# Optimization experiments

Hardware: AMD Instinct MI355X
Metric: run time of the kernel (lower is better)

The kernel has to match this reference:

```python
import jax, jax.numpy as jnp
import numpy as np


def _ln(x, g, b, eps=1e-5):
    mu = x.mean(-1, keepdims=True)
    var = ((x - mu) ** 2).mean(-1, keepdims=True)
    return (x - mu) / jnp.sqrt(var + eps) * g + b


def setup_inputs() -> dict:
    key = jax.random.key(0)
    ks = jax.random.split(key, 12)
    B, H, W, nh = 32, 64, 64, 8
    L = H * W
    dim, ffn_dim, mem_dim = 512, 2048, 512
    s = 0.02
    d = {}
    d["query"] = jax.random.normal(ks[0], (B, 1, dim), jnp.float32)
    d["mem"] = jax.random.normal(ks[1], (B, L, mem_dim), jnp.float32)
    d["ior_embs"] = jax.random.uniform(ks[2], (B, nh, H, W), jnp.float32)
    # input_proj: Linear(mem_dim, dim) + ReLU + LayerNorm(dim)
    d["W_in"] = jax.random.normal(ks[3], (mem_dim, dim), jnp.float32) * s
    d["b_in"] = jnp.zeros((dim,), jnp.float32)
    d["g_in"] = jnp.ones((dim,), jnp.float32)
    d["be_in"] = jnp.zeros((dim,), jnp.float32)
    # q_w: Linear(dim, dim); kv_w: Linear(dim, 2*dim)
    d["Wq"] = jax.random.normal(ks[4], (dim, dim), jnp.float32) * s
    d["bq"] = jnp.zeros((dim,), jnp.float32)
    d["Wkv"] = jax.random.normal(ks[5], (dim, 2 * dim), jnp.float32) * s
    d["bkv"] = jnp.zeros((2 * dim,), jnp.float32)
    # ffn: Mlp(dim, ffn_dim, dim) with GELU (exact)
    d["W1"] = jax.random.normal(ks[6], (dim, ffn_dim), jnp.float32) * s
    d["b1"] = jnp.zeros((ffn_dim,), jnp.float32)
    d["W2"] = jax.random.normal(ks[7], (ffn_dim, dim), jnp.float32) * s
    d["b2"] = jnp.zeros((dim,), jnp.float32)
    # norm_q, norm_ffn LayerNorms
    d["g_q"] = jnp.ones((dim,), jnp.float32)
    d["be_q"] = jnp.zeros((dim,), jnp.float32)
    d["g_f"] = jnp.ones((dim,), jnp.float32)
    d["be_f"] = jnp.zeros((dim,), jnp.float32)
    return d


def reference(query, mem, ior_embs, W_in, b_in, g_in, be_in, Wq, bq, Wkv, bkv,
              W1, b1, W2, b2, g_q, be_q, g_f, be_f):
    # input_proj: Linear + ReLU + LayerNorm
    m = _ln(jax.nn.relu(mem @ W_in + b_in), g_in, be_in)  # [B,L,C]
    B, L, C = m.shape
    nh = ior_embs.shape[1]
    h = C // nh
    scale = h ** -0.5
    ior = ior_embs.reshape(B, nh, L)  # flatten(2)
    kv = m @ Wkv + bkv
    k, v = kv[..., :C], kv[..., C:]
    # per-head split along last dim == reshape to [.., nh, h]
    q = (_ln(query, g_q, be_q) @ Wq + bq).reshape(B, 1, nh, h)
    k = k.reshape(B, L, nh, h)
    v = v.reshape(B, L, nh, h)
    # softmax-free attention gated by ior mask: attn = (q@k^T)*scale*ior
    attn = jnp.einsum('bqhd,blhd->bhql', q, k) * scale * ior[:, :, None, :]  # [B,nh,1,L]
    x = jnp.einsum('bhql,blhd->bqhd', attn, v).reshape(B, 1, C)  # concat heads
    x = x + query  # residual (short_cut)
    # FFN with pre-norm; dropout p=0 -> identity
    hdn = jax.nn.gelu(_ln(x, g_f, be_f) @ W1 + b1, approximate=False)
    x = x + (hdn @ W2 + b2)
    return x
```

## Files before the change

### kernel.cpp

```cpp
#include <hip/hip_runtime.h>
#include <hip/hip_bf16.h>
#include <math.h>

typedef unsigned short u16;
typedef __bf16 bf16x8 __attribute__((ext_vector_type(8)));
typedef float f32x4 __attribute__((ext_vector_type(4)));

__device__ __forceinline__ float b2f(u16 u) {
  union { unsigned int i; float f; } v; v.i = ((unsigned int)u) << 16; return v.f;
}
__device__ __forceinline__ u16 f2b(float f) {
  union { float f; unsigned int i; } v; v.f = f;
  unsigned int x = v.i;
  return (u16)((x + 0x7fffu + ((x >> 16) & 1u)) >> 16);
}
__device__ __forceinline__ float ldx(const void* p, size_t i, int isf) {
  return isf ? ((const float*)p)[i] : b2f(((const u16*)p)[i]);
}

__global__ void k_detect(const void* __restrict__ query, int* __restrict__ flag) {
  int t = threadIdx.x;
  float v = ((const float*)query)[t];
  int ok = (v == v && fabsf(v) < 100.f && fabsf(v) > 1e-4f) ? 1 : 0;
  unsigned long long m = __ballot(ok);
  if (t == 0) flag[0] = (__popcll(m) >= 32) ? 1 : 0;
}

__global__ __launch_bounds__(256) void k_makeB(const void* __restrict__ Win,
                                               u16* __restrict__ WTf,
                                               const int* __restrict__ flag) {
  int isf = flag[0];
  int t = threadIdx.x;
  int bx = blockIdx.x & 7, by = blockIdx.x >> 3;
  int k0 = bx * 64, j0 = by * 64;
  __shared__ float tile[64][65];
  #pragma unroll
  for (int kx = 0; kx < 16; kx++) {
    int idx = t + 256 * kx;
    int kl = idx >> 6, jl = idx & 63;
    tile[kl][jl] = ldx(Win, (size_t)(k0 + kl) * 512 + (j0 + jl), isf);
  }
  __syncthreads();
  #pragma unroll
  for (int i = 0; i < 2; i++) {
    int chunk = i * 256 + t;
    int q  = chunk & 3;
    int l  = (chunk >> 2) & 15;
    int ksL = (chunk >> 6) & 1;
    int jbL = (chunk >> 7) & 3;
    int j_local = jbL * 16 + l;
    int k_local = ksL * 32 + q * 8;
    union { u16 h[8]; uint4 u; } pk;
    #pragma unroll
    for (int r = 0; r < 8; r++) pk.h[r] = f2b(tile[k_local + r][j_local]);
    int jb = by * 4 + jbL, ks = bx * 2 + ksL;
    *(uint4*)(WTf + ((size_t)(jb * 16 + ks) * 16 + l) * 32 + q * 8) = pk.u;
  }
}

__global__ __launch_bounds__(512) void k_prep2(const void* __restrict__ Wkv,
                                               const void* __restrict__ g_in,
                                               const void* __restrict__ be_in,
                                               float* __restrict__ P1, float* __restrict__ P2,
                                               const int* __restrict__ flag) {
  int isf = flag[0];
  int blk = blockIdx.x;
  int t = threadIdx.x;
  int jj = t & 31, cg = t >> 5;
  int j = blk * 32 + jj;
  float p1 = 0.f, p2 = 0.f;
  for (int cc = 0; cc < 32; cc++) {
    int c = cg * 32 + cc;
    float wv = ldx(Wkv, (size_t)c * 1024 + 512 + j, isf);
    p1 += ldx(g_in, c, isf) * wv;
    p2 += ldx(be_in, c, isf) * wv;
  }
  __shared__ float red[1024];
  red[t * 2] = p1; red[t * 2 + 1] = p2;
  __syncthreads();
  if (t < 32) {
    float s1 = 0.f, s2 = 0.f;
    for (int g2 = 0; g2 < 16; g2++) { s1 += red[(g2 * 32 + t) * 2]; s2 += red[(g2 * 32 + t) * 2 + 1]; }
    P1[blk * 32 + t] = s1;
    P2[blk * 32 + t] = s2;
  }
}

__global__ __launch_bounds__(256) void k_qprep_a(
    const void* __restrict__ query, const void* __restrict__ Wq, const void* __restrict__ bq,
    const void* __restrict__ g_q, const void* __restrict__ be_q,
    float* __restrict__ qr_ws, const int* __restrict__ flag) {
  int isf = flag[0];
  int b = blockIdx.x, jq = blockIdx.y, t = threadIdx.x;
  __shared__ float qf[512];
  __shared__ float red[8];
  __shared__ float stats[2];

  float s = 0.f, ss = 0.f;
  for (int k = 0; k < 2; k++) {
    int c = t + 256 * k;
    float v = ldx(query, (size_t)b * 512 + c, isf);
    qf[c] = v; s += v; ss += v * v;
  }
  for (int off = 32; off; off >>= 1) { s += __shfl_xor(s, off); ss += __shfl_xor(ss, off); }
  int wid = t >> 6, lane = t & 63;
  if (lane == 0) { red[wid * 2] = s; red[wid * 2 + 1] = ss; }
  __syncthreads();
  if (t == 0) {
    float S = 0.f, SS = 0.f;
    for (int w = 0; w < 4; w++) { S += red[w * 2]; SS += red[w * 2 + 1]; }
    float mu = S / 512.f;
    float var = SS / 512.f - mu * mu;
    stats[0] = mu; stats[1] = rsqrtf(var + 1e-5f);
  }
  __syncthreads();
  float mu = stats[0], rstd = stats[1];
  for (int k = 0; k < 2; k++) {
    int c = t + 256 * k;
    qf[c] = (qf[c] - mu) * rstd * ldx(g_q, c, isf) + ldx(be_q, c, isf);
  }
  __syncthreads();
  int jl = t >> 1, half = t & 1;
  int j = jq * 128 + jl;
  const float* qh = qf + half * 256;
  float a0 = 0.f, a1 = 0.f, a2 = 0.f, a3 = 0.f;
  if (isf) {
    const float* wp = (const float*)Wq + (size_t)(half * 256) * 512 + j;
    #pragma unroll 2
    for (int cc = 0; cc < 256; cc += 4) {
      a0 += qh[cc]     * wp[(size_t)cc * 512];
      a1 += qh[cc + 1] * wp[(size_t)(cc + 1) * 512];
      a2 += qh[cc + 2] * wp[(size_t)(cc + 2) * 512];
      a3 += qh[cc + 3] * wp[(size_t)(cc + 3) * 512];
    }
  } else {
    const u16* wp = (const u16*)Wq + (size_t)(half * 256) * 512 + j;
    #pragma unroll 2
    for (int cc = 0; cc < 256; cc += 4) {
      a0 += qh[cc]     * b2f(wp[(size_t)cc * 512]);
      a1 += qh[cc + 1] * b2f(wp[(size_t)(cc + 1) * 512]);
      a2 += qh[cc + 2] * b2f(wp[(size_t)(cc + 2) * 512]);
      a3 += qh[cc + 3] * b2f(wp[(size_t)(cc + 3) * 512]);
    }
  }
  float acc = (a0 + a1) + (a2 + a3);
  acc += __shfl_xor(acc, 1);
  if (half == 0) qr_ws[(size_t)b * 512 + j] = acc + ldx(bq, j, isf);
}

__global__ __launch_bounds__(256) void k_qprep_b(
    const float* __restrict__ qr_ws, const void* __restrict__ Wkv, const void* __restrict__ bkv,
    const void* __restrict__ g_in, const void* __restrict__ be_in,
    u16* __restrict__ guT, float* __restrict__ Gsum_g, float* __restrict__ S0_g,
    const int* __restrict__ flag) {
  int isf = flag[0];
  int b = blockIdx.x, cq = blockIdx.y, t = threadIdx.x;
  __shared__ float qrl[512];
  __shared__ float ul[128 * 8];
  qrl[t] = qr_ws[(size_t)b * 512 + t];
  qrl[t + 256] = qr_ws[(size_t)b * 512 + t + 256];
  __syncthreads();
  #pragma unroll
  for (int e4 = 0; e4 < 4; e4++) {
    int e = t + 256 * e4;
    int cl = e >> 3, n = e & 7;
    int c = cq * 128 + cl;
    const float* qp = qrl + n * 64;
    float acc = 0.f;
    if (isf) {
      const float* wp = (const float*)Wkv + (size_t)c * 1024 + n * 64;
      #pragma unroll 8
      for (int d = 0; d < 64; d++) acc += wp[d] * qp[d];
    } else {
      const u16* wp = (const u16*)Wkv + (size_t)c * 1024 + n * 64;
      #pragma unroll 8
      for (int d = 0; d < 64; d++) acc += b2f(wp[d]) * qp[d];
    }
    ul[cl * 8 + n] = acc;
  }
  __syncthreads();
  #pragma unroll
  for (int e4 = 0; e4 < 4; e4++) {
    int e = t + 256 * e4;
    int cl = e >> 3, n = e & 7;
    int c = cq * 128 + cl;
    guT[((size_t)b * 16 + n) * 512 + c] = f2b(ldx(g_in, c, isf) * ul[cl * 8 + n]);
    guT[((size_t)b * 16 + 8 + n) * 512 + c] = 0;
  }
  if (t < 64) {
    int n = t >> 3, seg = t & 7;
    float gs = 0.f, s0 = 0.f;
    for (int k = 0; k < 16; k++) {
      int cl = seg * 16 + k;
      int c = cq * 128 + cl;
      float uu = ul[cl * 8 + n];
      gs += ldx(g_in, c, isf) * uu;
      s0 += ldx(be_in, c, isf) * uu;
    }
    gs += __shfl_xor(gs, 1); s0 += __shfl_xor(s0, 1);
    gs += __shfl_xor(gs, 2); s0 += __shfl_xor(s0, 2);
    gs += __shfl_xor(gs, 4); s0 += __shfl_xor(s0, 4);
    if (seg == 0) {
      atomicAdd(Gsum_g + b * 8 + n, gs);
      atomicAdd(S0_g + b * 8 + n, s0);
    }
  }
  if (cq == 0 && t < 8) {
    float acc = 0.f;
    for (int d = 0; d < 64; d++) acc += ldx(bkv, t * 64 + d, isf) * qrl[t * 64 + d];
    atomicAdd(S0_g + b * 8 + t, acc);
  }
}

#define LDA 40
__global__ __launch_bounds__(512) void k_main(
    const void* __restrict__ mem, const u16* __restrict__ WTf, const void* __restrict__ b_in,
    const void* __restrict__ ior, const u16* __restrict__ guT,
    const float* __restrict__ Gsum_g, const float* __restrict__ S0_g,
    float* __restrict__ R_g, float* __restrict__ A_g, float* __restrict__ M_g,
    const int* __restrict__ flag) {
  int isf = flag[0];
  int blk = blockIdx.x;
  int b   = blockIdx.y;
  int t = threadIdx.x;
  int w = t >> 6, lane = t & 63;
  int l15 = lane & 15, q = lane >> 4;

  __shared__ __align__(16) char smem[68096];
  u16*   Ab      = (u16*)smem;
  float* rowred  = (float*)smem;
  float* mu_rstd = (float*)(smem + 65536);
  float* a_lds   = (float*)(smem + 66048);
  char*  ymine   = smem + w * 8192;

  float binv[4];
  #pragma unroll
  for (int j = 0; j < 4; j++) binv[j] = ldx(b_in, w * 64 + j * 16 + l15, isf);
  bf16x8 gfrag0 = *(const bf16x8*)(guT + ((size_t)b * 16 + l15) * 512 + w * 64 + q * 8);
  bf16x8 gfrag1 = *(const bf16x8*)(guT + ((size_t)b * 16 + l15) * 512 + w * 64 + 32 + q * 8);
  float Gs  = Gsum_g[b * 8 + (t & 7)];
  float S0v = S0_g[b * 8 + (t & 7)];
  const u16* wb = WTf + (size_t)w * 32768 + l15 * 32 + q * 8;

  float am_acc = 0.f, mm_acc = 0.f;

  for (int tile = 0; tile < 4; tile++) {
    int row0 = (blk * 4 + tile) * 64;
    size_t memBase = ((size_t)b * 4096 + row0) * 512;

    f32x4 acc[4][4];
    #pragma unroll
    for (int i = 0; i < 4; i++)
      #pragma unroll
      for (int j = 0; j < 4; j++) { acc[i][j][0]=0.f; acc[i][j][1]=0.f; acc[i][j][2]=0.f; acc[i][j][3]=0.f; }

    for (int kk = 0; kk < 512; kk += 32) {
      __syncthreads();
      if (isf) {
        int e = t * 4;
        int r = e >> 5, c = e & 31;
        float4 v = *(const float4*)((const float*)mem + memBase + (size_t)r * 512 + kk + c);
        union { u16 h[4]; uint2 u; } pk;
        pk.h[0] = f2b(v.x); pk.h[1] = f2b(v.y); pk.h[2] = f2b(v.z); pk.h[3] = f2b(v.w);
        *(uint2*)(Ab + r * LDA + c) = pk.u;
      } else if (t < 256) {
        int r = t >> 2, ch = t & 3;
        uint4 v = *(const uint4*)((const u16*)mem + memBase + (size_t)r * 512 + kk + ch * 8);
        *(uint4*)(Ab + r * LDA + ch * 8) = v;
      }
      __syncthreads();
      int ks = kk >> 5;
      bf16x8 aF[4], bF[4];
      #pragma unroll
      for (int j = 0; j < 4; j++)
        bF[j] = *(const bf16x8*)(wb + j * 8192 + ks * 512);
      #pragma unroll
      for (int i = 0; i < 4; i++)
        aF[i] = *(const bf16x8*)(Ab + (i * 16 + l15) * LDA + q * 8);
      #pragma unroll
      for (int i = 0; i < 4; i++)
        #pragma unroll
        for (int j = 0; j < 4; j++)
          acc[i][j] = __builtin_amdgcn_mfma_f32_16x16x32_bf16(aF[i], bF[j], acc[i][j], 0, 0, 0);
    }
    __syncthreads();

    #pragma unroll
    for (int i = 0; i < 4; i++)
      #pragma unroll
      for (int j = 0; j < 4; j++)
        #pragma unroll
        for (int r = 0; r < 4; r++) {
          float v = acc[i][j][r] + binv[j];
          acc[i][j][r] = v > 0.f ? v : 0.f;
        }
    #pragma unroll
    for (int i = 0; i < 4; i++)
      #pragma unroll
      for (int r = 0; r < 4; r++) {
        float s  = acc[i][0][r] + acc[i][1][r] + acc[i][2][r] + acc[i][3][r];
        float ss = acc[i][0][r]*acc[i][0][r] + acc[i][1][r]*acc[i][1][r]
                 + acc[i][2][r]*acc[i][2][r] + acc[i][3][r]*acc[i][3][r];
        #pragma unroll
        for (int m = 1; m < 16; m <<= 1) { s += __shfl_xor(s, m); ss += __shfl_xor(ss, m); }
        if (l15 == 0) {
          int row = i * 16 + q * 4 + r;
          rowred[(w * 64 + row) * 2]     = s;
          rowred[(w * 64 + row) * 2 + 1] = ss;
        }
      }
    __syncthreads();
    if (t < 64) {
      float S = 0.f, SS = 0.f;
      for (int w2 = 0; w2 < 8; w2++) { S += rowred[(w2 * 64 + t) * 2]; SS += rowred[(w2 * 64 + t) * 2 + 1]; }
      float mu = S / 512.f;
      float var = SS / 512.f - mu * mu;
      mu_rstd[t * 2] = mu;
      mu_rstd[t * 2 + 1] = rsqrtf(var + 1e-5f);
    }
    __syncthreads();

    #pragma unroll
    for (int i = 0; i < 4; i++)
      #pragma unroll
      for (int j = 0; j < 4; j++)
        #pragma unroll
        for (int r = 0; r < 4; r++) {
          int row = i * 16 + q * 4 + r;
          int byo = (row * 128 + j * 32 + l15 * 2) ^ ((row & 7) << 4);
          *(u16*)(ymine + byo) = f2b(acc[i][j][r]);
        }
    __syncthreads();

    f32x4 Tacc[4];
    #pragma unroll
    for (int rt = 0; rt < 4; rt++) { Tacc[rt][0]=0.f; Tacc[rt][1]=0.f; Tacc[rt][2]=0.f; Tacc[rt][3]=0.f; }
    #pragma unroll
    for (int rt = 0; rt < 4; rt++) {
      int row = rt * 16 + l15;
      int sw = (row & 7) << 4;
      bf16x8 ay0 = *(const bf16x8*)(ymine + ((row * 128 + q * 16) ^ sw));
      Tacc[rt] = __builtin_amdgcn_mfma_f32_16x16x32_bf16(ay0, gfrag0, Tacc[rt], 0, 0, 0);
      bf16x8 ay1 = *(const bf16x8*)(ymine + ((row * 128 + 64 + q * 16) ^ sw));
      Tacc[rt] = __builtin_amdgcn_mfma_f32_16x16x32_bf16(ay1, gfrag1, Tacc[rt], 0, 0, 0);
    }
    {
      float* tp = (float*)ymine;
      if (l15 < 8) {
        #pragma unroll
        for (int rt = 0; rt < 4; rt++)
          #pragma unroll
          for (int r = 0; r < 4; r++)
            tp[(rt * 16 + q * 4 + r) * 8 + l15] = Tacc[rt][r];
      }
    }
    __syncthreads();

    {
      int row = t >> 3, n = t & 7;
      float Tsum = 0.f;
      #pragma unroll
      for (int w2 = 0; w2 < 8; w2++)
        Tsum += ((const float*)(smem + w2 * 8192))[row * 8 + n];
      float mu = mu_rstd[row * 2], rstd = mu_rstd[row * 2 + 1];
      float spre = rstd * (Tsum - mu * Gs) + S0v;
      float aval = spre * 0.125f * ldx(ior, ((size_t)b * 8 + n) * 4096 + row0 + row, isf);
      am_acc += aval;
      mm_acc += aval * mu * rstd;
      a_lds[row * 8 + n] = aval * rstd;
    }
    __syncthreads();

    float rv[4][8];
    #pragma unroll
    for (int j = 0; j < 4; j++)
      #pragma unroll
      for (int n = 0; n < 8; n++) rv[j][n] = 0.f;
    #pragma unroll
    for (int i = 0; i < 4; i++)
      #pragma unroll
      for (int r = 0; r < 4; r++) {
        int row = i * 16 + q * 4 + r;
        const float* ap = a_lds + row * 8;
        float a0=ap[0],a1=ap[1],a2=ap[2],a3=ap[3],a4=ap[4],a5=ap[5],a6=ap[6],a7=ap[7];
        #pragma unroll
        for (int j = 0; j < 4; j++) {
          float m = acc[i][j][r];
          rv[j][0] += m*a0; rv[j][1] += m*a1; rv[j][2] += m*a2; rv[j][3] += m*a3;
          rv[j][4] += m*a4; rv[j][5] += m*a5; rv[j][6] += m*a6; rv[j][7] += m*a7;
        }
      }
    #pragma unroll
    for (int j = 0; j < 4; j++)
      #pragma unroll
      for (int n = 0; n < 8; n++) {
        float v = rv[j][n];
        v += __shfl_xor(v, 16);
        v += __shfl_xor(v, 32);
        rv[j][n] = v;
      }
    if (q == 0) {
      #pragma unroll
      for (int j = 0; j < 4; j++)
        #pragma unroll
        for (int n = 0; n < 8; n++)
          atomicAdd(R_g + ((size_t)b * 8 + n) * 512 + (w * 64 + j * 16 + l15), rv[j][n]);
    }
  }

  am_acc += __shfl_xor(am_acc, 8);
  am_acc += __shfl_xor(am_acc, 16);
  am_acc += __shfl_xor(am_acc, 32);
  mm_acc += __shfl_xor(mm_acc, 8);
  mm_acc += __shfl_xor(mm_acc, 16);
  mm_acc += __shfl_xor(mm_acc, 32);
  if (lane < 8) {
    atomicAdd(A_g + b * 8 + lane, am_acc);
    atomicAdd(M_g + b * 8 + lane, mm_acc);
  }
}

__global__ __launch_bounds__(512) void k_mid(
    const float* __restrict__ R_g, const float* __restrict__ A_g, const float* __restrict__ M_g,
    const float* __restrict__ P1, const float* __restrict__ P2,
    const void* __restrict__ Wkv, const void* __restrict__ bkv, const void* __restrict__ g_in,
    const void* __restrict__ query, const void* __restrict__ g_f, const void* __restrict__ be_f,
    float* __restrict__ xrow_ws, float* __restrict__ xln_ws, float* __restrict__ y_acc,
    const int* __restrict__ flag) {
  int isf = flag[0];
  int b = blockIdx.x, t = threadIdx.x;
  __shared__ float Rl[4096];
  __shared__ float red[16];
  __shared__ float stats[2];
  #pragma unroll
  for (int k = 0; k < 8; k++) {
    int e = t + 512 * k;
    Rl[e] = R_g[(size_t)b * 4096 + e] * ldx(g_in, e & 511, isf);
  }
  __syncthreads();
  int j = t, n = t >> 6;
  float Av = A_g[b * 8 + n], Mv = M_g[b * 8 + n];
  float base = Av * ldx(bkv, 512 + j, isf) - Mv * P1[j] + Av * P2[j];
  const float* rl = Rl + n * 512;
  float a0 = 0.f, a1 = 0.f, a2 = 0.f, a3 = 0.f;
  if (isf) {
    const float* wv = (const float*)Wkv + 512 + j;
    #pragma unroll 2
    for (int c = 0; c < 512; c += 4) {
      a0 += rl[c]     * wv[(size_t)c * 1024];
      a1 += rl[c + 1] * wv[(size_t)(c + 1) * 1024];
      a2 += rl[c + 2] * wv[(size_t)(c + 2) * 1024];
      a3 += rl[c + 3] * wv[(size_t)(c + 3) * 1024];
    }
  } else {
    const u16* wv = (const u16*)Wkv + 512 + j;
    #pragma unroll 2
    for (int c = 0; c < 512; c += 4) {
      a0 += rl[c]     * b2f(wv[(size_t)c * 1024]);
      a1 += rl[c + 1] * b2f(wv[(size_t)(c + 1) * 1024]);
      a2 += rl[c + 2] * b2f(wv[(size_t)(c + 2) * 1024]);
      a3 += rl[c + 3] * b2f(wv[(size_t)(c + 3) * 1024]);
    }
  }
  float v = base + (a0 + a1) + (a2 + a3) + ldx(query, (size_t)b * 512 + t, isf);
  xrow_ws[(size_t)b * 512 + t] = v;
  y_acc[(size_t)b * 512 + t] = 0.f;
  float s1 = v, s2 = v * v;
  for (int off = 32; off; off >>= 1) { s1 += __shfl_xor(s1, off); s2 += __shfl_xor(s2, off); }
  int wid = t >> 6, lane = t & 63;
  if (lane == 0) { red[wid * 2] = s1; red[wid * 2 + 1] = s2; }
  __syncthreads();
  if (t == 0) {
    float S = 0.f, SS = 0.f;
    for (int w = 0; w < 8; w++) { S += red[w * 2]; SS += red[w * 2 + 1]; }
    float mu = S / 512.f;
    float var = SS / 512.f - mu * mu;
    stats[0] = mu; stats[1] = rsqrtf(var + 1e-5f);
  }
  __syncthreads();
  xln_ws[(size_t)b * 512 + t] = (v - stats[0]) * stats[1] * ldx(g_f, t, isf) + ldx(be_f, t, isf);
}

__global__ __launch_bounds__(512) void k_ffn12(
    const float* __restrict__ xln_ws, const void* __restrict__ W1, const void* __restrict__ b1,
    const void* __restrict__ W2, float* __restrict__ y_acc, const int* __restrict__ flag) {
  int isf = flag[0];
  int jb = blockIdx.x, b = blockIdx.y, t = threadIdx.x;
  __shared__ float xl[512];
  __shared__ float hl[512];
  xl[t] = xln_ws[(size_t)b * 512 + t];
  __syncthreads();
  int j = jb * 512 + t;
  float a0 = 0.f, a1 = 0.f, a2 = 0.f, a3 = 0.f;
  if (isf) {
    const float* wp = (const float*)W1 + j;
    #pragma unroll 2
    for (int c = 0; c < 512; c += 4) {
      a0 += xl[c]     * wp[(size_t)c * 2048];
      a1 += xl[c + 1] * wp[(size_t)(c + 1) * 2048];
      a2 += xl[c + 2] * wp[(size_t)(c + 2) * 2048];
      a3 += xl[c + 3] * wp[(size_t)(c + 3) * 2048];
    }
  } else {
    const u16* wp = (const u16*)W1 + j;
    #pragma unroll 2
    for (int c = 0; c < 512; c += 4) {
      a0 += xl[c]     * b2f(wp[(size_t)c * 2048]);
      a1 += xl[c + 1] * b2f(wp[(size_t)(c + 1) * 2048]);
      a2 += xl[c + 2] * b2f(wp[(size_t)(c + 2) * 2048]);
      a3 += xl[c + 3] * b2f(wp[(size_t)(c + 3) * 2048]);
    }
  }
  float acc = (a0 + a1) + (a2 + a3) + ldx(b1, j, isf);
  hl[t] = 0.5f * acc * (1.0f + erff(acc * 0.70710678118654752f));
  __syncthreads();
  float s0 = 0.f, s1 = 0.f, s2 = 0.f, s3 = 0.f;
  if (isf) {
    const float* wp = (const float*)W2 + (size_t)jb * 512 * 512 + t;
    #pragma unroll 2
    for (int c = 0; c < 512; c += 4) {
      s0 += hl[c]     * wp[(size_t)c * 512];
      s1 += hl[c + 1] * wp[(size_t)(c + 1) * 512];
      s2 += hl[c + 2] * wp[(size_t)(c + 2) * 512];
      s3 += hl[c + 3] * wp[(size_t)(c + 3) * 512];
    }
  } else {
    const u16* wp = (const u16*)W2 + (size_t)jb * 512 * 512 + t;
    #pragma unroll 2
    for (int c = 0; c < 512; c += 4) {
      s0 += hl[c]     * b2f(wp[(size_t)c * 512]);
      s1 += hl[c + 1] * b2f(wp[(size_t)(c + 1) * 512]);
      s2 += hl[c + 2] * b2f(wp[(size_t)(c + 2) * 512]);
      s3 += hl[c + 3] * b2f(wp[(size_t)(c + 3) * 512]);
    }
  }
  atomicAdd(y_acc + (size_t)b * 512 + t, (s0 + s1) + (s2 + s3));
}

__global__ __launch_bounds__(512) void k_final(
    const float* __restrict__ y_acc, const void* __restrict__ b2v,
    const float* __restrict__ xrow_ws, void* __restrict__ out,
    const int* __restrict__ flag) {
  int isf = flag[0];
  int b = blockIdx.x, t = threadIdx.x;
  float v = y_acc[(size_t)b * 512 + t] + ldx(b2v, t, isf) + xrow_ws[(size_t)b * 512 + t];
  if (isf) ((float*)out)[b * 512 + t] = v;
  else     ((u16*)out)[b * 512 + t] = f2b(v);
}

extern "C" void kernel_launch(void* const* d_in, const int* in_sizes, int n_in,
                              void* d_out, int out_size, void* d_ws, size_t ws_size,
                              hipStream_t stream) {
  const void* query = d_in[0];
  const void* mem   = d_in[1];
  const void* ior   = d_in[2];
  const void* W_in  = d_in[3];
  const void* b_in  = d_in[4];
  const void* g_in  = d_in[5];
  const void* be_in = d_in[6];
  const void* Wq    = d_in[7];
  const void* bq    = d_in[8];
  const void* Wkv   = d_in[9];
  const void* bkv   = d_in[10];
  const void* W1    = d_in[11];
  const void* b1    = d_in[12];
  const void* W2    = d_in[13];
  const void* b2v   = d_in[14];
  const void* g_q   = d_in[15];
  const void* be_q  = d_in[16];
  const void* g_f   = d_in[17];
  const void* be_f  = d_in[18];

  char* ws = (char*)d_ws;
  int*   flag   = (int*)ws;
  float* S0_g   = (float*)(ws + 256);
  float* Gsum_g = (float*)(ws + 1280);
  float* A_g    = (float*)(ws + 2304);
  float* M_g    = (float*)(ws + 3328);
  float* R_g    = (float*)(ws + 4352);
  u16*   guT    = (u16*)(ws + 528640);
  float* y_acc  = (float*)(ws + 528640);
  float* xrow_ws= (float*)(ws + 594176);
  float* xln_ws = (float*)(ws + 659712);
  u16*   WTf    = (u16*)(ws + 1052928);
  float* P1     = (float*)(ws + 1577216);
  float* P2     = (float*)(ws + 1579264);
  float* qr_ws  = (float*)(ws + 1581312);

  hipMemsetAsync(ws + 256, 0, 528384, stream);
  k_detect<<<dim3(1), dim3(64), 0, stream>>>(query, flag);
  k_makeB<<<dim3(64), dim3(256), 0, stream>>>(W_in, WTf, flag);
  k_prep2<<<dim3(16), dim3(512), 0, stream>>>(Wkv, g_in, be_in, P1, P2, flag);
  k_qprep_a<<<dim3(32, 4), dim3(256), 0, stream>>>(query, Wq, bq, g_q, be_q, qr_ws, flag);
  k_qprep_b<<<dim3(32, 4), dim3(256), 0, stream>>>(qr_ws, Wkv, bkv, g_in, be_in,
                                                   guT, Gsum_g, S0_g, flag);
  k_main<<<dim3(16, 32), dim3(512), 0, stream>>>(mem, WTf, b_in, ior, guT, Gsum_g, S0_g,
                                                 R_g, A_g, M_g, flag);
  k_mid<<<dim3(32), dim3(512), 0, stream>>>(R_g, A_g, M_g, P1, P2, Wkv, bkv, g_in,
                                            query, g_f, be_f, xrow_ws, xln_ws, y_acc, flag);
  k_ffn12<<<dim3(4, 32), dim3(512), 0, stream>>>(xln_ws, W1, b1, W2, y_acc, flag);
  k_final<<<dim3(32), dim3(512), 0, stream>>>(y_acc, b2v, xrow_ws, d_out, flag);
}
```

Before: 811.2 us.

## Stage full 64x512 mem tile in swizzled LDS once per tile

Instead of loading a 64x32 slice of mem into LDS and syncing twice for each of 16 k-steps, each tile now loads the whole 64x512 bf16 block (64KB) into LDS in one batched pass, with an XOR swizzle to avoid bank conflicts. The k-loop then reads only from LDS with no barriers. This removes per-step sync overhead and lets more global loads be in flight at once. In exchange it uses more registers for the batched loads, and no loads overlap with MFMA inside a tile.

```diff
diff --git a/kernel.cpp b/kernel.cpp
--- a/kernel.cpp
+++ b/kernel.cpp
@@ -212,7 +212,7 @@
   }
 }
 
-#define LDA 40
+#define LDSWZ(row, byte_in_row) ((((row) << 10) + (byte_in_row)) ^ (((row) & 7) << 4))
 __global__ __launch_bounds__(512) void k_main(
     const void* __restrict__ mem, const u16* __restrict__ WTf, const void* __restrict__ b_in,
     const void* __restrict__ ior, const u16* __restrict__ guT,
@@ -227,7 +227,6 @@
   int l15 = lane & 15, q = lane >> 4;
 
   __shared__ __align__(16) char smem[68096];
-  u16*   Ab      = (u16*)smem;
   float* rowred  = (float*)smem;
   float* mu_rstd = (float*)(smem + 65536);
   float* a_lds   = (float*)(smem + 66048);
@@ -248,35 +247,58 @@
     int row0 = (blk * 4 + tile) * 64;
     size_t memBase = ((size_t)b * 4096 + row0) * 512;
 
+    if (isf) {
+      #pragma unroll
+      for (int h = 0; h < 2; h++) {
+        float4 va[8];
+        #pragma unroll
+        for (int p = 0; p < 8; p++) {
+          int i16 = (h * 8 + p) * 512 + t;
+          va[p] = *(const float4*)((const float*)mem + memBase + (size_t)i16 * 4);
+        }
+        #pragma unroll
+        for (int p = 0; p < 8; p++) {
+          int i16 = (h * 8 + p) * 512 + t;
+          int row = i16 >> 7;
+          union { u16 hh[4]; uint2 u; } pk;
+          pk.hh[0] = f2b(va[p].x); pk.hh[1] = f2b(va[p].y);
+          pk.hh[2] = f2b(va[p].z); pk.hh[3] = f2b(va[p].w);
+          *(uint2*)(smem + LDSWZ(row, (i16 & 127) << 3)) = pk.u;
+        }
+      }
+    } else {
+      uint4 vb[8];
+      #pragma unroll
+      for (int p = 0; p < 8; p++) {
+        int i16 = p * 512 + t;
+        vb[p] = *(const uint4*)((const u16*)mem + memBase + (size_t)i16 * 8);
+      }
+      #pragma unroll
+      for (int p = 0; p < 8; p++) {
+        int i16 = p * 512 + t;
+        int row = i16 >> 6;
+        *(uint4*)(smem + LDSWZ(row, (i16 & 63) << 4)) = vb[p];
+      }
+    }
+    __syncthreads();
+
     f32x4 acc[4][4];
     #pragma unroll
     for (int i = 0; i < 4; i++)
       #pragma unroll
       for (int j = 0; j < 4; j++) { acc[i][j][0]=0.f; acc[i][j][1]=0.f; acc[i][j][2]=0.f; acc[i][j][3]=0.f; }
 
-    for (int kk = 0; kk < 512; kk += 32) {
-      __syncthreads();
-      if (isf) {
-        int e = t * 4;
-        int r = e >> 5, c = e & 31;
-        float4 v = *(const float4*)((const float*)mem + memBase + (size_t)r * 512 + kk + c);
-        union { u16 h[4]; uint2 u; } pk;
-        pk.h[0] = f2b(v.x); pk.h[1] = f2b(v.y); pk.h[2] = f2b(v.z); pk.h[3] = f2b(v.w);
-        *(uint2*)(Ab + r * LDA + c) = pk.u;
-      } else if (t < 256) {
-        int r = t >> 2, ch = t & 3;
-        uint4 v = *(const uint4*)((const u16*)mem + memBase + (size_t)r * 512 + kk + ch * 8);
-        *(uint4*)(Ab + r * LDA + ch * 8) = v;
-      }
-      __syncthreads();
-      int ks = kk >> 5;
+    #pragma unroll 4
+    for (int ks = 0; ks < 16; ks++) {
       bf16x8 aF[4], bF[4];
       #pragma unroll
       for (int j = 0; j < 4; j++)
         bF[j] = *(const bf16x8*)(wb + j * 8192 + ks * 512);
       #pragma unroll
-      for (int i = 0; i < 4; i++)
-        aF[i] = *(const bf16x8*)(Ab + (i * 16 + l15) * LDA + q * 8);
+      for (int i = 0; i < 4; i++) {
+        int row = i * 16 + l15;
+        aF[i] = *(const bf16x8*)(smem + LDSWZ(row, (ks << 6) + (q << 4)));
+      }
       #pragma unroll
       for (int i = 0; i < 4; i++)
         #pragma unroll
```

Result: faster. 761.7 us (-6.1%).
